# Kernel tuning notes

Hardware: AMD Instinct MI355X
Metric: run time of the kernel (lower is better)

## Reference

```python
import jax, jax.numpy as jnp
import numpy as np

B, N, D = 64, 2048, 256
EPS = 1e-05


def setup_inputs() -> dict:
    key = jax.random.key(0)
    k1, k2 = jax.random.split(key)
    x = jax.random.normal(k1, (B, N, D), dtype=jnp.float32)
    lengths = jax.random.randint(k2, (B,), 1, N + 1, dtype=jnp.int32)
    weights = jnp.ones((D,), dtype=jnp.float32)
    biases = jnp.zeros((D,), dtype=jnp.float32)
    return {"x": x, "lengths": lengths, "weights": weights, "biases": biases}


def reference(x, lengths, weights, biases):
    # mask: [B, N, 1], 1.0 for valid set elements (idx < length)
    mask = (jnp.arange(N)[None, :] < lengths[:, None])[..., None].astype(x.dtype)
    denom = (lengths.astype(x.dtype) * D)  # [B]
    xm = x * mask
    means = jnp.sum(xm, axis=(1, 2)) / denom                      # [B]
    x_centered = (xm - means[:, None, None]) * mask               # [B,N,D]
    variances = jnp.sum(x_centered * x_centered, axis=(1, 2)) / denom  # [B]
    x_norm = x_centered / (jnp.sqrt(variances)[:, None, None] + EPS)
    # F.linear(x, diag_embed(w), b) == x * w + b (elementwise per-feature affine)
    out = (x_norm * weights + biases) * mask
    return out
```

## Files before the change

kernel.cpp:

```cpp
#include <hip/hip_runtime.h>


#define BB 64
#define NN 2048
#define DD 256
#define EPSV 1e-5f
#define CHUNKS 32
#define GROUPS (NN / 4)
#define BAT4 (NN * DD / 4)
#define K2_BPB (GROUPS / 4)

typedef float f32x4 __attribute__((ext_vector_type(4)));

__global__ __launch_bounds__(256) void setnorm_partials(
    const float* __restrict__ x, const int* __restrict__ lengths,
    float* __restrict__ partials) {
  const int c = blockIdx.x;
  const int b = blockIdx.y;
  const int len = lengths[b];
  const int tRow = threadIdx.x >> 6;
  const int g4 = (len + 3) >> 2;
  int nk = (g4 - c + 31) >> 5;
  if (nk < 0) nk = 0;

  float sum = 0.f, sumsq = 0.f;
  const f32x4* px = (const f32x4*)x + (size_t)b * BAT4;
  #pragma unroll 4
  for (int k = 0; k < nk; ++k) {
    const int g = c + (k << 5);
    const f32x4 v = px[g * 256 + threadIdx.x];
    const int row = (g << 2) + tRow;
    if (row < len) {
      sum += v.x + v.y + v.z + v.w;
      sumsq += v.x * v.x + v.y * v.y + v.z * v.z + v.w * v.w;
    }
  }
  #pragma unroll
  for (int off = 32; off > 0; off >>= 1) {
    sum += __shfl_down(sum, off, 64);
    sumsq += __shfl_down(sumsq, off, 64);
  }
  __shared__ float ssum[4], ssq[4];
  const int wave = threadIdx.x >> 6;
  const int lane = threadIdx.x & 63;
  if (lane == 0) { ssum[wave] = sum; ssq[wave] = sumsq; }
  __syncthreads();
  if (threadIdx.x == 0) {
    const float ts = ssum[0] + ssum[1] + ssum[2] + ssum[3];
    const float tq = ssq[0] + ssq[1] + ssq[2] + ssq[3];
    partials[(b * CHUNKS + c) * 2 + 0] = ts;
    partials[(b * CHUNKS + c) * 2 + 1] = tq;
  }
}

__global__ __launch_bounds__(64) void setnorm_finalize(
    const int* __restrict__ lengths, float* __restrict__ partials) {
  const int b = blockIdx.x;
  float s = 0.f, q = 0.f;
  if (threadIdx.x < CHUNKS) {
    s = partials[(b * CHUNKS + threadIdx.x) * 2 + 0];
    q = partials[(b * CHUNKS + threadIdx.x) * 2 + 1];
  }
  #pragma unroll
  for (int off = 16; off > 0; off >>= 1) {
    s += __shfl_down(s, off, 64);
    q += __shfl_down(q, off, 64);
  }
  if (threadIdx.x == 0) {
    const float denom = (float)lengths[b] * (float)DD;
    const float mean = s / denom;
    float var = q / denom - mean * mean;
    var = fmaxf(var, 0.f);
    partials[b * CHUNKS * 2 + 0] = mean;
    partials[b * CHUNKS * 2 + 1] = 1.f / (sqrtf(var) + EPSV);
  }
}

__global__ __launch_bounds__(256) void setnorm_norm(
    const float* __restrict__ x, const int* __restrict__ lengths,
    const float* __restrict__ weights, const float* __restrict__ biases,
    const float* __restrict__ partials, float* __restrict__ out) {
  const int blk = blockIdx.x;
  const int b = blk >> 7;
  const int j = blk & 127;
  const int len = lengths[b];
  const float mean = partials[b * CHUNKS * 2 + 0];
  const float inv = partials[b * CHUNKS * 2 + 1];

  const int d4 = threadIdx.x & 63;
  const f32x4 w = ((const f32x4*)weights)[d4];
  const f32x4 bi = ((const f32x4*)biases)[d4];
  const int tRow = threadIdx.x >> 6;

  const f32x4* px = (const f32x4*)x + (size_t)b * BAT4;
  f32x4* po = (f32x4*)out + (size_t)b * BAT4;
  #pragma unroll
  for (int i = 0; i < 4; ++i) {
    const int g = j + (i << 7);
    const int idx4 = g * 256 + threadIdx.x;
    const int row = (g << 2) + tRow;
    f32x4 o = {0.f, 0.f, 0.f, 0.f};
    if (row < len) {
      const f32x4 v = px[idx4];
      o.x = (v.x - mean) * inv * w.x + bi.x;
      o.y = (v.y - mean) * inv * w.y + bi.y;
      o.z = (v.z - mean) * inv * w.z + bi.z;
      o.w = (v.w - mean) * inv * w.w + bi.w;
    }
    __builtin_nontemporal_store(o, po + idx4);
  }
}

extern "C" void kernel_launch(void* const* d_in, const int* in_sizes, int n_in,
                              void* d_out, int out_size, void* d_ws, size_t ws_size,
                              hipStream_t stream) {
  const float* x = (const float*)d_in[0];
  const int* lengths = (const int*)d_in[1];
  const float* weights = (const float*)d_in[2];
  const float* biases = (const float*)d_in[3];
  float* out = (float*)d_out;

  float* partials = (float*)d_ws;

  dim3 g1(CHUNKS, BB);
  setnorm_partials<<<g1, 256, 0, stream>>>(x, lengths, partials);
  setnorm_finalize<<<BB, 64, 0, stream>>>(lengths, partials);
  setnorm_norm<<<BB * K2_BPB, 256, 0, stream>>>(x, lengths, weights, biases,
                                                partials, out);
}
```

Before: 226.5 us.

## Fuse finalize into normalize kernel and move padded-row zeroing into stats pass

```diff
diff --git a/kernel.cpp b/kernel.cpp
--- a/kernel.cpp
+++ b/kernel.cpp
@@ -8,33 +8,54 @@
 #define CHUNKS 32
 #define GROUPS (NN / 4)
 #define BAT4 (NN * DD / 4)
-#define K2_BPB (GROUPS / 4)
+#define K2_BPB 128
 
 typedef float f32x4 __attribute__((ext_vector_type(4)));
 
-__global__ __launch_bounds__(256) void setnorm_partials(
+__global__ __launch_bounds__(256) void setnorm_pass1(
     const float* __restrict__ x, const int* __restrict__ lengths,
-    float* __restrict__ partials) {
+    float* __restrict__ partials, float* __restrict__ out) {
   const int c = blockIdx.x;
   const int b = blockIdx.y;
   const int len = lengths[b];
   const int tRow = threadIdx.x >> 6;
+  const f32x4* px = (const f32x4*)x + (size_t)b * BAT4;
+  f32x4* po = (f32x4*)out + (size_t)b * BAT4;
+
+  const int gFull = len >> 2;
   const int g4 = (len + 3) >> 2;
-  int nk = (g4 - c + 31) >> 5;
-  if (nk < 0) nk = 0;
+  int nFull = (gFull - c + 31) >> 5; if (nFull < 0) nFull = 0;
+  int kZ = (g4 - c + 31) >> 5;       if (kZ < 0) kZ = 0;
 
   float sum = 0.f, sumsq = 0.f;
-  const f32x4* px = (const f32x4*)x + (size_t)b * BAT4;
   #pragma unroll 4
-  for (int k = 0; k < nk; ++k) {
+  for (int k = 0; k < nFull; ++k) {
     const int g = c + (k << 5);
     const f32x4 v = px[g * 256 + threadIdx.x];
-    const int row = (g << 2) + tRow;
+    sum += v.x + v.y + v.z + v.w;
+    sumsq += v.x * v.x + v.y * v.y + v.z * v.z + v.w * v.w;
+  }
+  if ((len & 3) && ((gFull & 31) == c)) {
+    const int idx = gFull * 256 + threadIdx.x;
+    const int row = (gFull << 2) + tRow;
     if (row < len) {
+      const f32x4 v = px[idx];
       sum += v.x + v.y + v.z + v.w;
       sumsq += v.x * v.x + v.y * v.y + v.z * v.z + v.w * v.w;
+    } else {
+      const f32x4 z = {0.f, 0.f, 0.f, 0.f};
+      __builtin_nontemporal_store(z, po + idx);
     }
   }
+  {
+    const f32x4 z = {0.f, 0.f, 0.f, 0.f};
+    #pragma unroll 4
+    for (int k = kZ; k < 16; ++k) {
+      const int g = c + (k << 5);
+      __builtin_nontemporal_store(z, po + g * 256 + threadIdx.x);
+    }
+  }
+
   #pragma unroll
   for (int off = 32; off > 0; off >>= 1) {
     sum += __shfl_down(sum, off, 64);
@@ -53,30 +74,7 @@
   }
 }
 
-__global__ __launch_bounds__(64) void setnorm_finalize(
-    const int* __restrict__ lengths, float* __restrict__ partials) {
-  const int b = blockIdx.x;
-  float s = 0.f, q = 0.f;
-  if (threadIdx.x < CHUNKS) {
-    s = partials[(b * CHUNKS + threadIdx.x) * 2 + 0];
-    q = partials[(b * CHUNKS + threadIdx.x) * 2 + 1];
-  }
-  #pragma unroll
-  for (int off = 16; off > 0; off >>= 1) {
-    s += __shfl_down(s, off, 64);
-    q += __shfl_down(q, off, 64);
-  }
-  if (threadIdx.x == 0) {
-    const float denom = (float)lengths[b] * (float)DD;
-    const float mean = s / denom;
-    float var = q / denom - mean * mean;
-    var = fmaxf(var, 0.f);
-    partials[b * CHUNKS * 2 + 0] = mean;
-    partials[b * CHUNKS * 2 + 1] = 1.f / (sqrtf(var) + EPSV);
-  }
-}
-
-__global__ __launch_bounds__(256) void setnorm_norm(
+__global__ __launch_bounds__(256) void setnorm_pass2(
     const float* __restrict__ x, const int* __restrict__ lengths,
     const float* __restrict__ weights, const float* __restrict__ biases,
     const float* __restrict__ partials, float* __restrict__ out) {
@@ -84,8 +82,32 @@
   const int b = blk >> 7;
   const int j = blk & 127;
   const int len = lengths[b];
-  const float mean = partials[b * CHUNKS * 2 + 0];
-  const float inv = partials[b * CHUNKS * 2 + 1];
+  if ((j << 2) >= len) return;
+
+  __shared__ float s_mean, s_inv;
+  if (threadIdx.x < 64) {
+    float s = 0.f, q = 0.f;
+    if (threadIdx.x < CHUNKS) {
+      s = partials[(b * CHUNKS + threadIdx.x) * 2 + 0];
+      q = partials[(b * CHUNKS + threadIdx.x) * 2 + 1];
+    }
+    #pragma unroll
+    for (int off = 16; off > 0; off >>= 1) {
+      s += __shfl_down(s, off, 64);
+      q += __shfl_down(q, off, 64);
+    }
+    if (threadIdx.x == 0) {
+      const float denom = (float)len * (float)DD;
+      const float mean = s / denom;
+      float var = q / denom - mean * mean;
+      var = fmaxf(var, 0.f);
+      s_mean = mean;
+      s_inv = 1.f / (sqrtf(var) + EPSV);
+    }
+  }
+  __syncthreads();
+  const float mean = s_mean;
+  const float inv = s_inv;
 
   const int d4 = threadIdx.x & 63;
   const f32x4 w = ((const f32x4*)weights)[d4];
@@ -99,15 +121,15 @@
     const int g = j + (i << 7);
     const int idx4 = g * 256 + threadIdx.x;
     const int row = (g << 2) + tRow;
-    f32x4 o = {0.f, 0.f, 0.f, 0.f};
     if (row < len) {
       const f32x4 v = px[idx4];
+      f32x4 o;
       o.x = (v.x - mean) * inv * w.x + bi.x;
       o.y = (v.y - mean) * inv * w.y + bi.y;
       o.z = (v.z - mean) * inv * w.z + bi.z;
       o.w = (v.w - mean) * inv * w.w + bi.w;
+      __builtin_nontemporal_store(o, po + idx4);
     }
-    __builtin_nontemporal_store(o, po + idx4);
   }
 }
 
@@ -123,8 +145,7 @@
   float* partials = (float*)d_ws;
 
   dim3 g1(CHUNKS, BB);
-  setnorm_partials<<<g1, 256, 0, stream>>>(x, lengths, partials);
-  setnorm_finalize<<<BB, 64, 0, stream>>>(lengths, partials);
-  setnorm_norm<<<BB * K2_BPB, 256, 0, stream>>>(x, lengths, weights, biases,
-                                                partials, out);
+  setnorm_pass1<<<g1, 256, 0, stream>>>(x, lengths, partials, out);
+  setnorm_pass2<<<BB * K2_BPB, 256, 0, stream>>>(x, lengths, weights, biases,
+                                                 partials, out);
 }
```

Measured after the change: 232.4 us. 1.03x slower.
